# Performance work log

Measured on AMD Instinct MI355X. Metric: run time of the kernel, lower is better.

The kernel has to match this reference:

```python
import jax, jax.numpy as jnp
import numpy as np

N, M, D = 2048, 16, 256


def setup_inputs() -> dict:
    key = jax.random.key(0)
    k1, = jax.random.split(key, 1)
    embeddings = jax.random.normal(k1, (N, M, D), dtype=jnp.float32)
    w = jnp.asarray(10.0, dtype=jnp.float32)
    b = jnp.asarray(-5.0, dtype=jnp.float32)
    return {"embeddings": embeddings, "w": w, "b": b}


def reference(embeddings, w, b):
    # embeddings: [N, M, D]
    centroids = embeddings.mean(axis=1)          # [N, D]
    sum_ = embeddings.sum(axis=1)                # [N, D]
    e = embeddings.reshape(N * M, D)             # [NM, D]
    cosine_sim = e @ centroids.T                 # [NM, N]
    # excluded-self centroid for each (speaker j, utterance i):
    # cj = (sum_[j] - e_ji) / (M - 1); replace cosine_sim[ji, j] with dot(cj, e_ji)
    excl = (sum_[:, None, :] - embeddings) / (M - 1)           # [N, M, D]
    diag_vals = jnp.sum(excl * embeddings, axis=-1).reshape(N * M)  # [NM]
    labels = jnp.repeat(jnp.arange(N), M)                      # [NM]
    cosine_sim = cosine_sim.at[jnp.arange(N * M), labels].set(diag_vals)
    logits = w * cosine_sim + b                                # [NM, N]
    logp = jax.nn.log_softmax(logits, axis=-1)
    loss = -jnp.mean(logp[jnp.arange(N * M), labels])
    return loss
```

## Files before the change

### kernel.cpp

```cpp
#include <hip/hip_runtime.h>
#include <hip/hip_bf16.h>
#if !__has_builtin(__builtin_amdgcn_cvt_pk_fp8_f32)
#include <hip/hip_fp8.h>
#endif

#define NS 2048
#define MU 16
#define DD 256
#define NMROWS (NS*MU)
#define STRIPS 8
#define SC 256
#define NSTEP 8
#define BMROWS 128
#define THR 8.0f

typedef float  f32x4  __attribute__((ext_vector_type(4)));
typedef float  f32x16 __attribute__((ext_vector_type(16)));
typedef int    i32x4  __attribute__((ext_vector_type(4)));
typedef int    i32x8  __attribute__((ext_vector_type(8)));

#define LOG2E 1.44269504088896340736f
#define LN2   0.69314718055994530942f

#if __has_builtin(__builtin_amdgcn_exp2f)
#define EXP2F(x) __builtin_amdgcn_exp2f(x)
#else
#define EXP2F(x) exp2f(x)
#endif
#if __has_builtin(__builtin_amdgcn_logf)
#define LOG2F(x) __builtin_amdgcn_logf(x)
#else
#define LOG2F(x) __log2f(x)
#endif

__device__ __forceinline__ int pk4(float a, float b, float c, float d){
#if __has_builtin(__builtin_amdgcn_cvt_pk_fp8_f32)
  int v = __builtin_amdgcn_cvt_pk_fp8_f32(a, b, 0, false);
  v = __builtin_amdgcn_cvt_pk_fp8_f32(c, d, v, true);
  return v;
#else
  unsigned r = (unsigned)__hip_fp8_e4m3(a).__x
             | ((unsigned)__hip_fp8_e4m3(b).__x << 8)
             | ((unsigned)__hip_fp8_e4m3(c).__x << 16)
             | ((unsigned)__hip_fp8_e4m3(d).__x << 24);
  return (int)r;
#endif
}

__device__ __forceinline__ float max16(const f32x16& v){
  float t0 = fmaxf(fmaxf(v[0], v[1]), v[2]);
  float t1 = fmaxf(fmaxf(v[3], v[4]), v[5]);
  float t2 = fmaxf(fmaxf(v[6], v[7]), v[8]);
  float t3 = fmaxf(fmaxf(v[9], v[10]), v[11]);
  float t4 = fmaxf(fmaxf(v[12], v[13]), v[14]);
  return fmaxf(fmaxf(fmaxf(t0, t1), t2), fmaxf(fmaxf(t3, t4), v[15]));
}


__launch_bounds__(256)
__global__ void prep_kernel(const float* __restrict__ emb,
                            const float* __restrict__ wp,
                            i32x4* __restrict__ centk16,
                            unsigned char* __restrict__ embk8,
                            float* __restrict__ diag2){
  __shared__ float E[16*260];
  __shared__ float sm[256];
  const int t = threadIdx.x;
  const int n = blockIdx.x;
  const float* src = emb + (size_t)n*MU*DD;

  #pragma unroll
  for (int i=0;i<4;i++){
    int g = i*1024 + t*4;
    f32x4 v = *(const f32x4*)(src + g);
    int m = g >> 8, d = g & 255;
    *(f32x4*)&E[m*260 + d] = v;
  }
  __syncthreads();

  {
    float s = 0.f;
    #pragma unroll
    for (int m=0;m<16;m++) s += E[m*260 + t];
    sm[t] = s;
  }
  __syncthreads();

  const float w2 = wp[0] * LOG2E;

  if (t < 16){
    const float c16 = w2 * (1.0f/16.0f);
    const int st = t;
    const float* p = &sm[st*16];
    i32x4 o;
    #pragma unroll
    for (int q=0;q<4;q++)
      o[q] = pk4(p[q*4]*c16, p[q*4+1]*c16, p[q*4+2]*c16, p[q*4+3]*c16);
    centk16[(size_t)st*NS + n] = o;
  }

  if (embk8){
    int st = t >> 4, r = t & 15;
    const float* p = &E[r*260 + st*16];
    i32x4 o;
    #pragma unroll
    for (int q=0;q<4;q++){
      f32x4 v = *(const f32x4*)(p + q*4);
      o[q] = pk4(v[0], v[1], v[2], v[3]);
    }
    *(i32x4*)(embk8 + ((size_t)st*NMROWS + n*16 + r)*16) = o;
  }

  {
    int m = t >> 4, j = t & 15;
    float acc = 0.f;
    #pragma unroll
    for (int i=0;i<16;i++){
      int d = j + 16*i;
      float e = E[m*260 + d];
      acc += e * (sm[d] - e);
    }
    acc += __shfl_xor(acc, 1, 16);
    acc += __shfl_xor(acc, 2, 16);
    acc += __shfl_xor(acc, 4, 16);
    acc += __shfl_xor(acc, 8, 16);
    if (j==0) diag2[n*16 + m] = acc * (w2 * (1.0f/15.0f));
  }
}

__device__ __forceinline__ void stage_b(const i32x4* __restrict__ centk16,
                                        i32x4* lds, int col0,
                                        int wave, int lane){
  #pragma unroll
  for (int i=0;i<2;i++){
    const int st = i*8 + wave*2 + (lane >> 5);
    const i32x4* g = centk16 + (size_t)st*NS + col0 + (lane & 31);
    __builtin_amdgcn_global_load_lds(
        (const __attribute__((address_space(1))) void*)g,
        (__attribute__((address_space(3))) void*)(lds + (size_t)(i*8 + wave*2)*32),
        16, 0, 0);
  }
}

#define MFMAS(a,b,c) __builtin_amdgcn_mfma_scale_f32_32x32x64_f8f6f4( \
    a, b, c, 0, 0, 0, 0x7f7f7f7fu, 0, 0x7f7f7f7fu)

template<bool FROMF32>
__launch_bounds__(256,5)
__global__ void ge2e_main(const float* __restrict__ embf,
                          const unsigned char* __restrict__ embk8,
                          const i32x4* __restrict__ centk16,
                          const float* __restrict__ diag2,
                          float2* __restrict__ msbuf){
  __shared__ i32x4 Bbuf[2][512];

  const int tid  = threadIdx.x;
  const int lane = tid & 63;
  const int wave = tid >> 6;
  const int l31  = lane & 31, hi = lane >> 5;
  const int strip  = blockIdx.x & 7;
  const int rowBlk = blockIdx.x >> 3;
  const int c0 = strip * SC;
  const int rowA = rowBlk*BMROWS + wave*32 + l31;

  stage_b(centk16, &Bbuf[0][0], c0, wave, lane);

  i32x8 af[4];
  if constexpr (FROMF32){
    const float* rp = embf + (size_t)rowA*DD;
    #pragma unroll
    for (int c=0;c<4;c++){
      i32x8 o;
      #pragma unroll
      for (int h=0;h<2;h++){
        const float* q = rp + (4*c + 2*hi + h)*16;
        #pragma unroll
        for (int j=0;j<4;j++)
          o[h*4+j] = pk4(q[j*4], q[j*4+1], q[j*4+2], q[j*4+3]);
      }
      af[c] = o;
    }
  } else {
    #pragma unroll
    for (int c=0;c<4;c++){
      i32x4 x = *(const i32x4*)(embk8 + ((size_t)(4*c+2*hi  )*NMROWS + rowA)*16);
      i32x4 y = *(const i32x4*)(embk8 + ((size_t)(4*c+2*hi+1)*NMROWS + rowA)*16);
      i32x8 o; o[0]=x[0];o[1]=x[1];o[2]=x[2];o[3]=x[3];
               o[4]=y[0];o[5]=y[1];o[6]=y[2];o[7]=y[3];
      af[c] = o;
    }
  }

  const float dv  = diag2[rowA];
  const int   lab = rowA >> 4;
  const int   labc0 = rowBlk*8;
  const bool  hasdiag = (labc0 >= c0) && (labc0 < c0 + SC);
  const int   dstep = (labc0 - c0) >> 5;

  float m = -3.0e38f, s = 0.f;

  __syncthreads();

  for (int step=0; step<NSTEP; ++step){
    const int cb_ = step & 1;
    if (step+1 < NSTEP)
      stage_b(centk16, &Bbuf[cb_^1][0], c0 + (step+1)*32, wave, lane);

    const i32x4* cur = &Bbuf[cb_][0];

    f32x16 acc;
    #pragma unroll
    for (int i=0;i<16;i++) acc[i] = 0.f;

    #pragma unroll
    for (int c=0;c<4;c++){
      i32x4 x = cur[(4*c+2*hi  )*32 + l31];
      i32x4 y = cur[(4*c+2*hi+1)*32 + l31];
      i32x8 bb; bb[0]=x[0];bb[1]=x[1];bb[2]=x[2];bb[3]=x[3];
                bb[4]=y[0];bb[5]=y[1];bb[6]=y[2];bb[7]=y[3];
      acc = MFMAS(bb, af[c], acc);
    }

    if (hasdiag && step == dstep){
      int colbase = c0 + step*32 + 4*hi;
      #pragma unroll
      for (int r=0;r<16;r++){
        int col = colbase + (r&3) + 8*(r>>2);
        if (col == lab) acc[r] = dv;
      }
    }

    float tm = max16(acc);
    if (__any(tm > m + THR)){
      float mn = fmaxf(m, tm);
      s *= EXP2F(m - mn);
      m = mn;
    }
    float e0 = EXP2F(acc[0]-m)+EXP2F(acc[1]-m)+EXP2F(acc[2]-m)+EXP2F(acc[3]-m);
    float e1 = EXP2F(acc[4]-m)+EXP2F(acc[5]-m)+EXP2F(acc[6]-m)+EXP2F(acc[7]-m);
    float e2 = EXP2F(acc[8]-m)+EXP2F(acc[9]-m)+EXP2F(acc[10]-m)+EXP2F(acc[11]-m);
    float e3 = EXP2F(acc[12]-m)+EXP2F(acc[13]-m)+EXP2F(acc[14]-m)+EXP2F(acc[15]-m);
    s += (e0+e1)+(e2+e3);

    asm volatile("s_waitcnt vmcnt(0)" ::: "memory");
    __builtin_amdgcn_s_barrier();
  }

  float mo = __shfl_xor(m,32,64), so = __shfl_xor(s,32,64);
  float mm = fmaxf(m,mo);
  float ss = s*EXP2F(m-mm) + so*EXP2F(mo-mm);

  if (hi==0) msbuf[(size_t)strip*NMROWS + rowA] = make_float2(mm, ss);
}

__launch_bounds__(512)
__global__ void merge_kernel(const float2* __restrict__ msbuf,
                             const float* __restrict__ diag2,
                             float* __restrict__ partials){
  __shared__ float sh[8];
  const int row = blockIdx.x*512 + threadIdx.x;
  float2 p[STRIPS];
  #pragma unroll
  for (int k=0;k<STRIPS;k++) p[k] = msbuf[(size_t)k*NMROWS + row];
  float mm = p[0].x;
  #pragma unroll
  for (int k=1;k<STRIPS;k++) mm = fmaxf(mm, p[k].x);
  float ss = 0.f;
  #pragma unroll
  for (int k=0;k<STRIPS;k++) ss += p[k].y * EXP2F(p[k].x - mm);
  float term = LN2*(mm + LOG2F(ss) - diag2[row]);
  #pragma unroll
  for (int off=32; off; off>>=1) term += __shfl_xor(term, off, 64);
  if ((threadIdx.x & 63)==0) sh[threadIdx.x>>6] = term;
  __syncthreads();
  if (threadIdx.x==0){
    float v = 0.f;
    #pragma unroll
    for (int i=0;i<8;i++) v += sh[i];
    partials[blockIdx.x] = v;
  }
}

__global__ void final_kernel(const float* __restrict__ partials,
                             float* __restrict__ out){
  int tid = threadIdx.x;
  float v = partials[tid];
  #pragma unroll
  for (int off=32; off; off>>=1) v += __shfl_xor(v, off, 64);
  if (tid==0) out[0] = v * (1.0f/NMROWS);
}

extern "C" void kernel_launch(void* const* d_in, const int* in_sizes, int n_in,
                              void* d_out, int out_size, void* d_ws, size_t ws_size,
                              hipStream_t stream){
  const float* emb = (const float*)d_in[0];
  const float* wp  = (const float*)d_in[1];
  float* out = (float*)d_out;
  char* ws = (char*)d_ws;

  const size_t centk_b = (size_t)NS*DD;
  const size_t embk_b  = (size_t)NMROWS*DD;
  const size_t diag_b  = (size_t)NMROWS*4;
  const size_t ms_b    = (size_t)STRIPS*NMROWS*8;
  const bool useEmbk = ws_size >= centk_b + embk_b + diag_b + ms_b + 1024;

  i32x4* centk16 = (i32x4*)ws;
  size_t off = centk_b;
  unsigned char* embk8 = useEmbk ? (unsigned char*)(ws + off) : nullptr;
  if (useEmbk) off += embk_b;
  float*  diag2 = (float*)(ws + off);  off += diag_b;
  float2* msbuf = (float2*)(ws + off); off += ms_b;
  float*  parts = (float*)(ws + off);

  prep_kernel<<<NS, 256, 0, stream>>>(emb, wp, centk16, embk8, diag2);
  if (useEmbk)
    ge2e_main<false><<<(NMROWS/BMROWS)*STRIPS, 256, 0, stream>>>(emb, embk8, centk16, diag2, msbuf);
  else
    ge2e_main<true><<<(NMROWS/BMROWS)*STRIPS, 256, 0, stream>>>(emb, embk8, centk16, diag2, msbuf);
  merge_kernel<<<NMROWS/512, 512, 0, stream>>>(msbuf, diag2, parts);
  final_kernel<<<1, 64, 0, stream>>>(parts, out);
}
```

Before: 42.06 us.

## Fold running-max subtraction into MFMA accumulator init and fuse final reduction

The MFMA accumulator is now seeded with the negated running max, so the subtraction before each exp2 happens for free inside the matrix op and the common no-rescale path skips the per-element subtract. The final reduction kernel is folded into the merge kernel with an atomic last-block counter, which removes one launch but adds a memset of the counter. Launch bounds are loosened from 5 to 4 waves-per-SIMD, which may allow more registers at the cost of occupancy.

```diff
diff --git a/kernel.cpp b/kernel.cpp
--- a/kernel.cpp
+++ b/kernel.cpp
@@ -146,7 +146,7 @@
     a, b, c, 0, 0, 0, 0x7f7f7f7fu, 0, 0x7f7f7f7fu)
 
 template<bool FROMF32>
-__launch_bounds__(256,5)
+__launch_bounds__(256,4)
 __global__ void ge2e_main(const float* __restrict__ embf,
                           const unsigned char* __restrict__ embk8,
                           const i32x4* __restrict__ centk16,
@@ -197,7 +197,10 @@
   const bool  hasdiag = (labc0 >= c0) && (labc0 < c0 + SC);
   const int   dstep = (labc0 - c0) >> 5;
 
-  float m = -3.0e38f, s = 0.f;
+  float mneg = 0.f, s = 0.f;
+  f32x16 civ;
+  #pragma unroll
+  for (int i=0;i<16;i++) civ[i] = 0.f;
 
   __syncthreads();
 
@@ -209,16 +212,13 @@
     const i32x4* cur = &Bbuf[cb_][0];
 
     f32x16 acc;
-    #pragma unroll
-    for (int i=0;i<16;i++) acc[i] = 0.f;
-
     #pragma unroll
     for (int c=0;c<4;c++){
       i32x4 x = cur[(4*c+2*hi  )*32 + l31];
       i32x4 y = cur[(4*c+2*hi+1)*32 + l31];
       i32x8 bb; bb[0]=x[0];bb[1]=x[1];bb[2]=x[2];bb[3]=x[3];
                 bb[4]=y[0];bb[5]=y[1];bb[6]=y[2];bb[7]=y[3];
-      acc = MFMAS(bb, af[c], acc);
+      acc = MFMAS(bb, af[c], (c==0) ? civ : acc);
     }
 
     if (hasdiag && step == dstep){
@@ -226,26 +226,35 @@
       #pragma unroll
       for (int r=0;r<16;r++){
         int col = colbase + (r&3) + 8*(r>>2);
-        if (col == lab) acc[r] = dv;
+        if (col == lab) acc[r] = dv + mneg;
       }
     }
 
     float tm = max16(acc);
-    if (__any(tm > m + THR)){
-      float mn = fmaxf(m, tm);
-      s *= EXP2F(m - mn);
-      m = mn;
-    }
-    float e0 = EXP2F(acc[0]-m)+EXP2F(acc[1]-m)+EXP2F(acc[2]-m)+EXP2F(acc[3]-m);
-    float e1 = EXP2F(acc[4]-m)+EXP2F(acc[5]-m)+EXP2F(acc[6]-m)+EXP2F(acc[7]-m);
-    float e2 = EXP2F(acc[8]-m)+EXP2F(acc[9]-m)+EXP2F(acc[10]-m)+EXP2F(acc[11]-m);
-    float e3 = EXP2F(acc[12]-m)+EXP2F(acc[13]-m)+EXP2F(acc[14]-m)+EXP2F(acc[15]-m);
-    s += (e0+e1)+(e2+e3);
+    if (__any(tm > THR)){
+      float d = fmaxf(tm, 0.f);
+      s *= EXP2F(-d);
+      mneg -= d;
+      #pragma unroll
+      for (int i=0;i<16;i++) civ[i] = mneg;
+      float a0 = EXP2F(acc[0]-d)+EXP2F(acc[1]-d)+EXP2F(acc[2]-d)+EXP2F(acc[3]-d);
+      float a1 = EXP2F(acc[4]-d)+EXP2F(acc[5]-d)+EXP2F(acc[6]-d)+EXP2F(acc[7]-d);
+      float a2 = EXP2F(acc[8]-d)+EXP2F(acc[9]-d)+EXP2F(acc[10]-d)+EXP2F(acc[11]-d);
+      float a3 = EXP2F(acc[12]-d)+EXP2F(acc[13]-d)+EXP2F(acc[14]-d)+EXP2F(acc[15]-d);
+      s += (a0+a1)+(a2+a3);
+    } else {
+      float a0 = EXP2F(acc[0])+EXP2F(acc[1])+EXP2F(acc[2])+EXP2F(acc[3]);
+      float a1 = EXP2F(acc[4])+EXP2F(acc[5])+EXP2F(acc[6])+EXP2F(acc[7]);
+      float a2 = EXP2F(acc[8])+EXP2F(acc[9])+EXP2F(acc[10])+EXP2F(acc[11]);
+      float a3 = EXP2F(acc[12])+EXP2F(acc[13])+EXP2F(acc[14])+EXP2F(acc[15]);
+      s += (a0+a1)+(a2+a3);
+    }
 
     asm volatile("s_waitcnt vmcnt(0)" ::: "memory");
     __builtin_amdgcn_s_barrier();
   }
 
+  float m  = -mneg;
   float mo = __shfl_xor(m,32,64), so = __shfl_xor(s,32,64);
   float mm = fmaxf(m,mo);
   float ss = s*EXP2F(m-mm) + so*EXP2F(mo-mm);
@@ -256,9 +265,13 @@
 __launch_bounds__(512)
 __global__ void merge_kernel(const float2* __restrict__ msbuf,
                              const float* __restrict__ diag2,
-                             float* __restrict__ partials){
+                             float* __restrict__ partials,
+                             unsigned int* __restrict__ counter,
+                             float* __restrict__ out){
   __shared__ float sh[8];
-  const int row = blockIdx.x*512 + threadIdx.x;
+  __shared__ int last;
+  const int tid = threadIdx.x;
+  const int row = blockIdx.x*512 + tid;
   float2 p[STRIPS];
   #pragma unroll
   for (int k=0;k<STRIPS;k++) p[k] = msbuf[(size_t)k*NMROWS + row];
@@ -271,23 +284,24 @@
   float term = LN2*(mm + LOG2F(ss) - diag2[row]);
   #pragma unroll
   for (int off=32; off; off>>=1) term += __shfl_xor(term, off, 64);
-  if ((threadIdx.x & 63)==0) sh[threadIdx.x>>6] = term;
-  __syncthreads();
-  if (threadIdx.x==0){
+  if ((tid & 63)==0) sh[tid>>6] = term;
+  __syncthreads();
+  if (tid==0){
     float v = 0.f;
     #pragma unroll
     for (int i=0;i<8;i++) v += sh[i];
     partials[blockIdx.x] = v;
-  }
-}
-
-__global__ void final_kernel(const float* __restrict__ partials,
-                             float* __restrict__ out){
-  int tid = threadIdx.x;
-  float v = partials[tid];
-  #pragma unroll
-  for (int off=32; off; off>>=1) v += __shfl_xor(v, off, 64);
-  if (tid==0) out[0] = v * (1.0f/NMROWS);
+    __threadfence();
+    last = (atomicAdd(counter, 1u) == (unsigned)(gridDim.x - 1));
+  }
+  __syncthreads();
+  if (last && tid < 64){
+    __threadfence();
+    float v = partials[tid];
+    #pragma unroll
+    for (int off=32; off; off>>=1) v += __shfl_xor(v, off, 64);
+    if (tid==0) out[0] = v * (1.0f/NMROWS);
+  }
 }
 
 extern "C" void kernel_launch(void* const* d_in, const int* in_sizes, int n_in,
@@ -302,21 +316,22 @@
   const size_t embk_b  = (size_t)NMROWS*DD;
   const size_t diag_b  = (size_t)NMROWS*4;
   const size_t ms_b    = (size_t)STRIPS*NMROWS*8;
-  const bool useEmbk = ws_size >= centk_b + embk_b + diag_b + ms_b + 1024;
+  const bool useEmbk = ws_size >= centk_b + embk_b + diag_b + ms_b + 4096;
 
   i32x4* centk16 = (i32x4*)ws;
   size_t off = centk_b;
   unsigned char* embk8 = useEmbk ? (unsigned char*)(ws + off) : nullptr;
   if (useEmbk) off += embk_b;
-  float*  diag2 = (float*)(ws + off);  off += diag_b;
-  float2* msbuf = (float2*)(ws + off); off += ms_b;
-  float*  parts = (float*)(ws + off);
-
+  float*        diag2   = (float*)(ws + off);        off += diag_b;
+  float2*       msbuf   = (float2*)(ws + off);       off += ms_b;
+  float*        parts   = (float*)(ws + off);        off += 64*sizeof(float);
+  unsigned int* counter = (unsigned int*)(ws + off);
+
+  hipMemsetAsync(counter, 0, sizeof(unsigned int), stream);
   prep_kernel<<<NS, 256, 0, stream>>>(emb, wp, centk16, embk8, diag2);
   if (useEmbk)
     ge2e_main<false><<<(NMROWS/BMROWS)*STRIPS, 256, 0, stream>>>(emb, embk8, centk16, diag2, msbuf);
   else
     ge2e_main<true><<<(NMROWS/BMROWS)*STRIPS, 256, 0, stream>>>(emb, embk8, centk16, diag2, msbuf);
-  merge_kernel<<<NMROWS/512, 512, 0, stream>>>(msbuf, diag2, parts);
-  final_kernel<<<1, 64, 0, stream>>>(parts, out);
-}
+  merge_kernel<<<NMROWS/512, 512, 0, stream>>>(msbuf, diag2, parts, counter, out);
+}
```

After: 48.47 us. +15.2%, slower.
